# Performance work log

Measured on AMD Instinct MI355X. Metric: run time of the kernel, lower is better.

## Reference

```python
import jax, jax.numpy as jnp
import numpy as np

OUT_C, IN_C, KS, KN = 256, 256, 3, 4
TEMP = 1.0
D1 = OUT_C * KS            # 768
D2 = IN_C * KS             # 768
D2R = D2 // 2 + 1          # 385 (rfft width)


def _freq_indices():
    # mirror torch get_fft2freq(d1, d2, use_rfft=True)
    fh = np.fft.fftfreq(D1)
    fw = np.fft.rfftfreq(D2)
    grid = np.stack(np.meshgrid(fh, fw, indexing='ij'), axis=-1)  # (D1, D2R, 2)
    dist = np.linalg.norm(grid, axis=-1).ravel()
    idx = np.argsort(dist, kind='stable')
    return (idx // D2R).astype(np.int32), (idx % D2R).astype(np.int32)


def setup_inputs() -> dict:
    key = jax.random.key(0)
    k1, k2, k3 = jax.random.split(key, 3)
    b, h, w = 8, 64, 64
    fh, fw = _freq_indices()
    num_freq = fh.shape[0]  # 295680 = D1 * D2R (param_reduction == 1.0)
    return {
        'x': jax.random.normal(k1, (b, IN_C, h, w), dtype=jnp.float32),
        'dft_weight': jax.random.normal(k2, (KN, num_freq, 2), dtype=jnp.float32) * 1e-6,
        'k_att': jax.random.normal(k3, (b, KN, 1, 1), dtype=jnp.float32),
        'freq_h': jnp.asarray(fh),
        'freq_w': jnp.asarray(fw),
    }


def reference(x, dft_weight, k_att, freq_h, freq_w):
    b, c, h, w = x.shape
    # kernel attention: sigmoid(att / temp) * 2 / kernel_num
    att = jax.nn.sigmoid(k_att / TEMP) * (2.0 / KN)          # (b, KN, 1, 1)
    # weighted sum of per-kernel frequency weights -> (b, F, 2)
    wsum = jnp.einsum('knf,bk->bnf', dft_weight, att.reshape(b, KN))
    wc = jax.lax.complex(wsum[..., 0], wsum[..., 1])          # (b, F) complex
    # scatter into dense rfft2 map (indices are a permutation: no duplicates)
    dft_map = jnp.zeros((b, D1, D2R), dtype=jnp.complex64)
    dft_map = dft_map.at[:, freq_h, freq_w].set(wc)
    # inverse rFFT2 -> spatial weights (b, D1, D2)
    sw = jnp.fft.irfft2(dft_map, s=(D1, D2))
    # (b, out, ks, in, ks) -> (b, out, in, ks, ks) -> grouped-conv kernel
    wk = sw.reshape(b, OUT_C, KS, IN_C, KS).transpose(0, 1, 3, 2, 4)
    wk = wk.reshape(b * OUT_C, IN_C, KS, KS)
    # batch of per-sample convs == one grouped conv with groups=b
    xg = x.reshape(1, b * c, h, w)
    out = jax.lax.conv_general_dilated(
        xg, wk, window_strides=(1, 1), padding=[(1, 1), (1, 1)],
        dimension_numbers=('NCHW', 'OIHW', 'NCHW'), feature_group_count=b)
    return out.reshape(b, OUT_C, out.shape[2], out.shape[3])
```

## Files before the change

kernel.cpp:

```cpp
#include <hip/hip_runtime.h>
#include <math.h>

#define D1 768
#define D2R 385
#define NF 295680
#define KNUM 4
#define NB 8
#define NC 256
#define TWOPI_768 0.008181230868723419f

#define ATW_U32 1572864u
#define YA_U32 2752512u
#define T_U32 3981312u
#define SPECB_K_U32 344064u
#define WBF_BYTE 9437184u

typedef __attribute__((ext_vector_type(8))) short short8;
typedef __attribute__((ext_vector_type(16))) float f32x16;
union U4S8 { unsigned int u[4]; uint4 u4; short8 s8; };

static __device__ __forceinline__ unsigned int f2bf(float f) {
  unsigned int u = __float_as_uint(f);
  return (u + 0x7fffu + ((u >> 16) & 1u)) >> 16;
}

__global__ __launch_bounds__(256) void prep_kernel(
    const float* __restrict__ dw, const int* __restrict__ fh,
    const int* __restrict__ fw, unsigned int* __restrict__ ws) {
  long i = (long)blockIdx.x * 256 + threadIdx.x;
  if (i < 1182720) {
    int k = (int)(i / NF);
    int r = (int)(i - (long)k * NF);
    const float2 v = ((const float2*)dw)[i];
    int h = fh[r], c = fw[r];
    ws[(size_t)k * SPECB_K_U32 + (size_t)c * 768 + h] =
        f2bf(v.x) | (f2bf(v.y) << 16);
    return;
  }
  long j = i - 1182720;
  if (j < 1179648) {
    int ri = (int)(j / 589824);
    int rem = (int)(j - (long)ri * 589824);
    int m = rem / 768, h = rem - (rem / 768) * 768;
    int idx = (h * m) % 768;
    float s, c;
    sincosf((float)idx * TWOPI_768, &s, &c);
    unsigned lo, hi;
    if (ri == 0) { lo = f2bf(c); hi = f2bf(-s); }
    else         { lo = f2bf(s); hi = f2bf(c); }
    ws[ATW_U32 + j] = lo | (hi << 16);
  } else if (j < 1486848) {
    long p = j - 1179648;
    int n = (int)(p / 400), cc = (int)(p - (p / 400) * 400);
    unsigned v = 0;
    if (cc <= 384) {
      float wgt = (cc == 0 || cc == 384) ? 1.6954210069444445e-6f
                                         : 3.390842013888889e-6f;
      int idx = (cc * n) % 768;
      float s, c;
      sincosf((float)idx * TWOPI_768, &s, &c);
      v = f2bf(wgt * c) | (f2bf(-wgt * s) << 16);
    }
    ws[T_U32 + (size_t)n * 400 + cc] = v;
  } else if (j < 1680384) {
    long p = j - 1486848;
    int k = (int)(p / 48384);
    long r = p - (long)k * 48384;
    int row = 385 + (int)(r / 768);
    int col = (int)(r - (r / 768) * 768);
    ws[(size_t)k * SPECB_K_U32 + (size_t)row * 768 + col] = 0u;
  } else if (j < 1726464) {
    long p = j - 1680384;
    int k = (int)(p / 11520);
    long r = p - (long)k * 11520;
    int m = (int)(r / 15), jj = (int)(r - (r / 15) * 15);
    ws[YA_U32 + (size_t)k * 307200 + (size_t)m * 400 + 385 + jj] = 0u;
  }
}

__global__ __launch_bounds__(256) void fftA_kernel(
    const unsigned short* __restrict__ Atw,
    const unsigned short* __restrict__ specB,
    unsigned short* __restrict__ Ya) {
  __shared__ __align__(16) unsigned short Al[2][64 * 40], Bl[2][64 * 40];
  int t = threadIdx.x;
  int mt = blockIdx.x, nt = blockIdx.y, z = blockIdx.z;
  int ri = z & 1, k = z >> 1;
  const unsigned short* Ag =
      Atw + (size_t)ri * 1179648 + (size_t)(mt * 64) * 1536;
  const unsigned short* Bg =
      specB + (size_t)k * 688128 + (size_t)(nt * 64) * 1536;
  int rowS = t >> 2, q = t & 3;
  int lane = t & 63, w = t >> 6;
  int moff = (w & 1) * 32, noff = (w >> 1) * 32;
  int lm = lane & 31, half = lane >> 5;
  int wr = rowS * 40 + q * 8;
  int ao = (moff + lm) * 40 + half * 8;
  int bo = (noff + lm) * 40 + half * 8;

  f32x16 acc;
#pragma unroll
  for (int r = 0; r < 16; ++r) acc[r] = 0.f;

  uint4 av = *(const uint4*)(Ag + (size_t)rowS * 1536 + q * 8);
  uint4 bv = *(const uint4*)(Bg + (size_t)rowS * 1536 + q * 8);
  *(uint4*)&Al[0][wr] = av;
  *(uint4*)&Bl[0][wr] = bv;
  __syncthreads();

  for (int kb = 0; kb < 48; ++kb) {
    bool more = (kb < 47);
    if (more) {
      av = *(const uint4*)(Ag + (size_t)rowS * 1536 + (kb + 1) * 32 + q * 8);
      bv = *(const uint4*)(Bg + (size_t)rowS * 1536 + (kb + 1) * 32 + q * 8);
    }
    const unsigned short* Ab = Al[kb & 1];
    const unsigned short* Bb = Bl[kb & 1];
#pragma unroll
    for (int kk2 = 0; kk2 < 2; ++kk2) {
      short8 a8 = *(const short8*)&Ab[ao + kk2 * 16];
      short8 b8 = *(const short8*)&Bb[bo + kk2 * 16];
      acc = __builtin_amdgcn_mfma_f32_32x32x16_bf16(a8, b8, acc, 0, 0, 0);
    }
    if (more) {
      *(uint4*)&Al[(kb + 1) & 1][wr] = av;
      *(uint4*)&Bl[(kb + 1) & 1][wr] = bv;
    }
    __syncthreads();
  }

  int c = nt * 64 + noff + lm;
  if (c < D2R) {
    unsigned short* Yk = Ya + (size_t)k * 614400;
    int mb = mt * 64 + moff + 4 * half;
#pragma unroll
    for (int reg = 0; reg < 16; ++reg) {
      int m = mb + (reg & 3) + 8 * (reg >> 2);
      Yk[(size_t)m * 800 + 2 * c + ri] = (unsigned short)f2bf(acc[reg]);
    }
  }
}

__global__ __launch_bounds__(256) void fftB_kernel(
    const unsigned short* __restrict__ Ya, const unsigned short* __restrict__ T,
    float* __restrict__ SW) {
  __shared__ __align__(16) unsigned short Al[2][64 * 40], Bl[2][64 * 40];
  int t = threadIdx.x;
  int mt = blockIdx.x, nt = blockIdx.y, k = blockIdx.z;
  const unsigned short* Ag = Ya + (size_t)k * 614400 + (size_t)(mt * 64) * 800;
  const unsigned short* Bg = T + (size_t)(nt * 64) * 800;
  int rowS = t >> 2, q = t & 3;
  int lane = t & 63, w = t >> 6;
  int moff = (w & 1) * 32, noff = (w >> 1) * 32;
  int lm = lane & 31, half = lane >> 5;
  int wr = rowS * 40 + q * 8;
  int ao = (moff + lm) * 40 + half * 8;
  int bo = (noff + lm) * 40 + half * 8;

  f32x16 acc;
#pragma unroll
  for (int r = 0; r < 16; ++r) acc[r] = 0.f;

  uint4 av = *(const uint4*)(Ag + (size_t)rowS * 800 + q * 8);
  uint4 bv = *(const uint4*)(Bg + (size_t)rowS * 800 + q * 8);
  *(uint4*)&Al[0][wr] = av;
  *(uint4*)&Bl[0][wr] = bv;
  __syncthreads();

  for (int kb = 0; kb < 25; ++kb) {
    bool more = (kb < 24);
    if (more) {
      av = *(const uint4*)(Ag + (size_t)rowS * 800 + (kb + 1) * 32 + q * 8);
      bv = *(const uint4*)(Bg + (size_t)rowS * 800 + (kb + 1) * 32 + q * 8);
    }
    const unsigned short* Ab = Al[kb & 1];
    const unsigned short* Bb = Bl[kb & 1];
#pragma unroll
    for (int kk2 = 0; kk2 < 2; ++kk2) {
      short8 a8 = *(const short8*)&Ab[ao + kk2 * 16];
      short8 b8 = *(const short8*)&Bb[bo + kk2 * 16];
      acc = __builtin_amdgcn_mfma_f32_32x32x16_bf16(a8, b8, acc, 0, 0, 0);
    }
    if (more) {
      *(uint4*)&Al[(kb + 1) & 1][wr] = av;
      *(uint4*)&Bl[(kb + 1) & 1][wr] = bv;
    }
    __syncthreads();
  }

  float* SWk = SW + (size_t)k * 589824;
  int n = nt * 64 + noff + lm;
  int mb = mt * 64 + moff + 4 * half;
#pragma unroll
  for (int reg = 0; reg < 16; ++reg) {
    int m = mb + (reg & 3) + 8 * (reg >> 2);
    SWk[(size_t)m * 768 + n] = acc[reg];
  }
}

__global__ __launch_bounds__(256) void wprep_kernel(
    const float* __restrict__ ka, const float* __restrict__ SW,
    unsigned short* __restrict__ wBF) {
  __shared__ float rowL[4][768];
  int t = threadIdx.x;
  int row = blockIdx.x;
  int oc = row / 3, dy = row - oc * 3;
  if (t < 192) {
#pragma unroll
    for (int k = 0; k < 4; ++k)
      *(float4*)&rowL[k][t * 4] =
          *(const float4*)(SW + (size_t)k * 589824 + (size_t)row * 768 + t * 4);
  }
  float att[8][4];
#pragma unroll
  for (int b = 0; b < 8; ++b)
#pragma unroll
    for (int k = 0; k < 4; ++k)
      att[b][k] = 0.5f / (1.f + expf(-ka[b * 4 + k]));
  __syncthreads();
  int icb = t >> 4, i = t & 15;
#pragma unroll
  for (int dx = 0; dx < 3; ++dx) {
    int col = icb * 48 + dx + 3 * i;
    float v0 = rowL[0][col], v1 = rowL[1][col], v2 = rowL[2][col],
          v3 = rowL[3][col];
    int s = dy * 3 + dx;
#pragma unroll
    for (int b = 0; b < 8; ++b) {
      float v = att[b][0] * v0 + att[b][1] * v1 + att[b][2] * v2 +
                att[b][3] * v3;
      wBF[(((size_t)(b * 16 + icb) * 9 + s) * 256 + oc) * 16 + i] =
          (unsigned short)f2bf(v);
    }
  }
}

__global__ __launch_bounds__(256, 4) void conv_mfma_kernel(
    const float* __restrict__ x, const unsigned short* __restrict__ wBF,
    float* __restrict__ out) {
  __shared__ __align__(16) unsigned char ldsX[2][4 * 66 * 48];
  int t = threadIdx.x;
  int pxt = blockIdx.x, oct = blockIdx.y, b = blockIdx.z;
  int py0 = pxt * 2, oc0 = oct * 64;
  int lane = t & 63, w = t >> 6;
  int pxq = w & 1, pxw = w >> 1;
  int n = lane & 31, half = lane >> 5;

  if (t < 192) {
    int buf = t / 96, r2 = t - buf * 96;
    int site = r2 / 12, word = r2 - site * 12;
    int r = site >> 1, c = (site & 1) ? 65 : 0;
    *(unsigned int*)(&ldsX[buf][(r * 66 + c) * 48 + word * 4]) = 0u;
  }

  f32x16 acc[2];
#pragma unroll
  for (int i = 0; i < 2; ++i)
#pragma unroll
    for (int r = 0; r < 16; ++r) acc[i][r] = 0.f;

  int s_cq = t >> 5, s_r = (t >> 3) & 3, s_icp = t & 7;
  int iy = py0 - 1 + s_r;
  bool valid = (iy >= 0 && iy < 64);
  const float* xpb =
      x + (((size_t)b * NC) * 64 + (valid ? iy : 0)) * 64 + s_cq * 8;
  int xwoff = (s_r * 66 + 1 + s_cq * 8) * 48 + s_icp * 4;

  const uint4* wg4 = (const uint4*)wBF;
  size_t abase = (size_t)b * 144 * 512 + (size_t)(oc0 + n) * 2 + half;
  U4S8 pf[3][2];
#pragma unroll
  for (int i = 0; i < 3; ++i) {
    pf[i][0].u4 = wg4[abase + (size_t)i * 512];
    pf[i][1].u4 = wg4[abase + (size_t)i * 512 + 64];
  }

  {
    float4 qa0 = make_float4(0.f, 0.f, 0.f, 0.f), qa1 = qa0, qb0 = qa0,
           qb1 = qa0;
    if (valid) {
      const float* p0 = xpb + (size_t)(s_icp * 2) * 4096;
      qa0 = *(const float4*)p0;
      qa1 = *(const float4*)(p0 + 4);
      qb0 = *(const float4*)(p0 + 4096);
      qb1 = *(const float4*)(p0 + 4100);
    }
    float av[8] = {qa0.x, qa0.y, qa0.z, qa0.w, qa1.x, qa1.y, qa1.z, qa1.w};
    float bv[8] = {qb0.x, qb0.y, qb0.z, qb0.w, qb1.x, qb1.y, qb1.z, qb1.w};
    unsigned char* xw = &ldsX[0][0] + xwoff;
#pragma unroll
    for (int j = 0; j < 8; ++j)
      *(unsigned int*)(xw + j * 48) = f2bf(av[j]) | (f2bf(bv[j]) << 16);
  }
  __syncthreads();

  for (int icb = 0; icb < 16; ++icb) {
    float4 qa0 = make_float4(0.f, 0.f, 0.f, 0.f), qa1 = qa0, qb0 = qa0,
           qb1 = qa0;
    if (icb < 15 && valid) {
      const float* p0 = xpb + ((size_t)(icb + 1) * 16 + s_icp * 2) * 4096;
      qa0 = *(const float4*)p0;
      qa1 = *(const float4*)(p0 + 4);
      qb0 = *(const float4*)(p0 + 4096);
      qb1 = *(const float4*)(p0 + 4100);
    }
    const unsigned char* bufR = &ldsX[icb & 1][0];
#pragma unroll
    for (int s = 0; s < 9; ++s) {
      int step = icb * 9 + s;
      int slot = s % 3;
      int dy = s / 3, dx = s - dy * 3;
      const unsigned char* bb =
          bufR + ((pxq + dy) * 66 + pxw * 32 + n + dx) * 48 + half * 16;
      short8 B0 = *(const short8*)bb;
      acc[0] = __builtin_amdgcn_mfma_f32_32x32x16_bf16(pf[slot][0].s8, B0,
                                                       acc[0], 0, 0, 0);
      acc[1] = __builtin_amdgcn_mfma_f32_32x32x16_bf16(pf[slot][1].s8, B0,
                                                       acc[1], 0, 0, 0);
      if (step + 3 < 144) {
        pf[slot][0].u4 = wg4[abase + (size_t)(step + 3) * 512];
        pf[slot][1].u4 = wg4[abase + (size_t)(step + 3) * 512 + 64];
      }
    }
    if (icb < 15) {
      float av[8] = {qa0.x, qa0.y, qa0.z, qa0.w, qa1.x, qa1.y, qa1.z, qa1.w};
      float bv[8] = {qb0.x, qb0.y, qb0.z, qb0.w, qb1.x, qb1.y, qb1.z, qb1.w};
      unsigned char* xw = &ldsX[(icb + 1) & 1][0] + xwoff;
#pragma unroll
      for (int j = 0; j < 8; ++j)
        *(unsigned int*)(xw + j * 48) = f2bf(av[j]) | (f2bf(bv[j]) << 16);
    }
    __syncthreads();
  }

  int py = py0 + pxq;
  int pxc = pxw * 32 + n;
#pragma unroll
  for (int osub = 0; osub < 2; ++osub) {
    int OC = oc0 + osub * 32 + 4 * half;
    float* op = out + (((size_t)(b * NC + OC)) * 64 + py) * 64 + pxc;
#pragma unroll
    for (int reg = 0; reg < 16; ++reg) {
      int ocm = (reg & 3) + 8 * (reg >> 2);
      op[(size_t)ocm * 4096] = acc[osub][reg];
    }
  }
}

extern "C" void kernel_launch(void* const* d_in, const int* in_sizes, int n_in,
                              void* d_out, int out_size, void* d_ws,
                              size_t ws_size, hipStream_t stream) {
  const float* x = (const float*)d_in[0];
  const float* dw = (const float*)d_in[1];
  const float* ka = (const float*)d_in[2];
  const int* fh = (const int*)d_in[3];
  const int* fw = (const int*)d_in[4];
  float* out = (float*)d_out;
  unsigned int* ws = (unsigned int*)d_ws;
  const unsigned short* specB = (const unsigned short*)d_ws;
  const unsigned short* Atw = (const unsigned short*)((char*)d_ws + 6291456);
  unsigned short* Ya = (unsigned short*)((char*)d_ws + 11010048);
  const unsigned short* T = (const unsigned short*)((char*)d_ws + 15925248);
  float* SW = (float*)d_ws;
  unsigned short* wBF = (unsigned short*)((char*)d_ws + WBF_BYTE);

  hipLaunchKernelGGL(prep_kernel, dim3(11364), dim3(256), 0, stream, dw, fh,
                     fw, ws);
  hipLaunchKernelGGL(fftA_kernel, dim3(12, 7, 8), dim3(256), 0, stream, Atw,
                     specB, Ya);
  hipLaunchKernelGGL(fftB_kernel, dim3(12, 12, KNUM), dim3(256), 0, stream, Ya,
                     T, SW);
  hipLaunchKernelGGL(wprep_kernel, dim3(768), dim3(256), 0, stream, ka, SW,
                     wBF);
  hipLaunchKernelGGL(conv_mfma_kernel, dim3(32, 4, NB), dim3(256), 0, stream,
                     x, wBF, out);
}
```

Measured before the change: 217.0 us.

## Enlarge conv output tile to 128 channels and use hardware sin/cos in prep

The conv kernel now covers 128 output channels per block, with each wave computing a 64oc x 64px tile as 2x2 MFMAs, and the grid's channel dimension is halved. Each B fragment and weight fragment is reused twice, so every x tile is loaded and converted into LDS only half as often, and weight prefetch now runs a full icb (9 steps) ahead. This raises register pressure: four accumulators plus 18 prefetch registers, with launch bounds lowered to 2 blocks per SM. The twiddle-table generation also replaces sincosf with the hardware sin/cos intrinsics, which take revolutions and may be slightly less accurate.

Measured after the change: 193.2 us. 10.9% less time.

```diff
diff --git a/kernel.cpp b/kernel.cpp
--- a/kernel.cpp
+++ b/kernel.cpp
@@ -8,6 +8,7 @@
 #define NB 8
 #define NC 256
 #define TWOPI_768 0.008181230868723419f
+#define INV768 0.0013020833333333333f
 
 #define ATW_U32 1572864u
 #define YA_U32 2752512u
@@ -22,6 +23,13 @@
 static __device__ __forceinline__ unsigned int f2bf(float f) {
   unsigned int u = __float_as_uint(f);
   return (u + 0x7fffu + ((u >> 16) & 1u)) >> 16;
+}
+
+static __device__ __forceinline__ void sincos_rev768(int idx, float* s,
+                                                     float* c) {
+  float rev = (float)idx * INV768;
+  *s = __builtin_amdgcn_sinf(rev);
+  *c = __builtin_amdgcn_cosf(rev);
 }
 
 __global__ __launch_bounds__(256) void prep_kernel(
@@ -44,7 +52,7 @@
     int m = rem / 768, h = rem - (rem / 768) * 768;
     int idx = (h * m) % 768;
     float s, c;
-    sincosf((float)idx * TWOPI_768, &s, &c);
+    sincos_rev768(idx, &s, &c);
     unsigned lo, hi;
     if (ri == 0) { lo = f2bf(c); hi = f2bf(-s); }
     else         { lo = f2bf(s); hi = f2bf(c); }
@@ -58,7 +66,7 @@
                                          : 3.390842013888889e-6f;
       int idx = (cc * n) % 768;
       float s, c;
-      sincosf((float)idx * TWOPI_768, &s, &c);
+      sincos_rev768(idx, &s, &c);
       v = f2bf(wgt * c) | (f2bf(-wgt * s) << 16);
     }
     ws[T_U32 + (size_t)n * 400 + cc] = v;
@@ -235,15 +243,15 @@
   }
 }
 
-__global__ __launch_bounds__(256, 4) void conv_mfma_kernel(
+__global__ __launch_bounds__(256, 2) void conv_mfma_kernel(
     const float* __restrict__ x, const unsigned short* __restrict__ wBF,
     float* __restrict__ out) {
   __shared__ __align__(16) unsigned char ldsX[2][4 * 66 * 48];
   int t = threadIdx.x;
   int pxt = blockIdx.x, oct = blockIdx.y, b = blockIdx.z;
-  int py0 = pxt * 2, oc0 = oct * 64;
+  int py0 = pxt * 2, oc0 = oct * 128;
   int lane = t & 63, w = t >> 6;
-  int pxq = w & 1, pxw = w >> 1;
+  int ocq = w >> 1, pxq = w & 1;
   int n = lane & 31, half = lane >> 5;
 
   if (t < 192) {
@@ -253,11 +261,13 @@
     *(unsigned int*)(&ldsX[buf][(r * 66 + c) * 48 + word * 4]) = 0u;
   }
 
-  f32x16 acc[2];
+  f32x16 acc[2][2];
 #pragma unroll
   for (int i = 0; i < 2; ++i)
 #pragma unroll
-    for (int r = 0; r < 16; ++r) acc[i][r] = 0.f;
+    for (int j = 0; j < 2; ++j)
+#pragma unroll
+      for (int r = 0; r < 16; ++r) acc[i][j][r] = 0.f;
 
   int s_cq = t >> 5, s_r = (t >> 3) & 3, s_icp = t & 7;
   int iy = py0 - 1 + s_r;
@@ -267,10 +277,11 @@
   int xwoff = (s_r * 66 + 1 + s_cq * 8) * 48 + s_icp * 4;
 
   const uint4* wg4 = (const uint4*)wBF;
-  size_t abase = (size_t)b * 144 * 512 + (size_t)(oc0 + n) * 2 + half;
-  U4S8 pf[3][2];
-#pragma unroll
-  for (int i = 0; i < 3; ++i) {
+  size_t abase =
+      (size_t)b * 144 * 512 + (size_t)(oc0 + ocq * 64 + n) * 2 + half;
+  U4S8 pf[9][2];
+#pragma unroll
+  for (int i = 0; i < 9; ++i) {
     pf[i][0].u4 = wg4[abase + (size_t)i * 512];
     pf[i][1].u4 = wg4[abase + (size_t)i * 512 + 64];
   }
@@ -308,18 +319,22 @@
 #pragma unroll
     for (int s = 0; s < 9; ++s) {
       int step = icb * 9 + s;
-      int slot = s % 3;
       int dy = s / 3, dx = s - dy * 3;
       const unsigned char* bb =
-          bufR + ((pxq + dy) * 66 + pxw * 32 + n + dx) * 48 + half * 16;
+          bufR + ((pxq + dy) * 66 + n + dx) * 48 + half * 16;
       short8 B0 = *(const short8*)bb;
-      acc[0] = __builtin_amdgcn_mfma_f32_32x32x16_bf16(pf[slot][0].s8, B0,
-                                                       acc[0], 0, 0, 0);
-      acc[1] = __builtin_amdgcn_mfma_f32_32x32x16_bf16(pf[slot][1].s8, B0,
-                                                       acc[1], 0, 0, 0);
-      if (step + 3 < 144) {
-        pf[slot][0].u4 = wg4[abase + (size_t)(step + 3) * 512];
-        pf[slot][1].u4 = wg4[abase + (size_t)(step + 3) * 512 + 64];
+      short8 B1 = *(const short8*)(bb + 32 * 48);
+      acc[0][0] = __builtin_amdgcn_mfma_f32_32x32x16_bf16(pf[s][0].s8, B0,
+                                                          acc[0][0], 0, 0, 0);
+      acc[0][1] = __builtin_amdgcn_mfma_f32_32x32x16_bf16(pf[s][0].s8, B1,
+                                                          acc[0][1], 0, 0, 0);
+      acc[1][0] = __builtin_amdgcn_mfma_f32_32x32x16_bf16(pf[s][1].s8, B0,
+                                                          acc[1][0], 0, 0, 0);
+      acc[1][1] = __builtin_amdgcn_mfma_f32_32x32x16_bf16(pf[s][1].s8, B1,
+                                                          acc[1][1], 0, 0, 0);
+      if (icb < 15) {
+        pf[s][0].u4 = wg4[abase + (size_t)(step + 9) * 512];
+        pf[s][1].u4 = wg4[abase + (size_t)(step + 9) * 512 + 64];
       }
     }
     if (icb < 15) {
@@ -334,17 +349,19 @@
   }
 
   int py = py0 + pxq;
-  int pxc = pxw * 32 + n;
-#pragma unroll
-  for (int osub = 0; osub < 2; ++osub) {
-    int OC = oc0 + osub * 32 + 4 * half;
-    float* op = out + (((size_t)(b * NC + OC)) * 64 + py) * 64 + pxc;
-#pragma unroll
-    for (int reg = 0; reg < 16; ++reg) {
-      int ocm = (reg & 3) + 8 * (reg >> 2);
-      op[(size_t)ocm * 4096] = acc[osub][reg];
-    }
-  }
+#pragma unroll
+  for (int osub = 0; osub < 2; ++osub)
+#pragma unroll
+    for (int psub = 0; psub < 2; ++psub) {
+      int OC = oc0 + ocq * 64 + osub * 32 + 4 * half;
+      int pxc = psub * 32 + n;
+      float* op = out + (((size_t)(b * NC + OC)) * 64 + py) * 64 + pxc;
+#pragma unroll
+      for (int reg = 0; reg < 16; ++reg) {
+        int ocm = (reg & 3) + 8 * (reg >> 2);
+        op[(size_t)ocm * 4096] = acc[osub][psub][reg];
+      }
+    }
 }
 
 extern "C" void kernel_launch(void* const* d_in, const int* in_sizes, int n_in,
@@ -372,6 +389,6 @@
                      T, SW);
   hipLaunchKernelGGL(wprep_kernel, dim3(768), dim3(256), 0, stream, ka, SW,
                      wBF);
-  hipLaunchKernelGGL(conv_mfma_kernel, dim3(32, 4, NB), dim3(256), 0, stream,
+  hipLaunchKernelGGL(conv_mfma_kernel, dim3(32, 2, NB), dim3(256), 0, stream,
                      x, wBF, out);
 }
```
